# Performance work log

Measured on AMD Instinct MI355X. Metric: run time of the kernel, lower is better.

The kernel has to match this reference:

```python
import jax, jax.numpy as jnp
import numpy as np

N = 100000   # nodes
E = 3200000  # edges
NC = 32


def cheb_conv(x, row, col, W, b):
    """PyG ChebConv with sym normalization and default lambda_max=2.
    Scaled Laplacian L_hat = 2L/lambda_max - I has zero diagonal and
    off-diagonal weights -d_i^{-1/2} d_j^{-1/2} (self-loops removed first).
    W: [K, in, out], b: [out] or None.
    """
    n = x.shape[0]
    ew = jnp.where(row != col, 1.0, 0.0).astype(x.dtype)  # remove_self_loops
    deg = jax.ops.segment_sum(ew, row, num_segments=n)
    dinv = jnp.where(deg > 0, jax.lax.rsqrt(jnp.maximum(deg, 1e-12)), 0.0)
    w = -ew * dinv[row] * dinv[col]  # [E] edge weights of L_hat

    def L(v):  # L_hat @ v via gather + segment-sum scatter
        return jax.ops.segment_sum(w[:, None] * v[col], row, num_segments=n)

    K = W.shape[0]
    Tx0 = x
    out = Tx0 @ W[0]
    if K > 1:
        Tx1 = L(x)
        out = out + Tx1 @ W[1]
        for k in range(2, K):  # Chebyshev recurrence T_k = 2 L T_{k-1} - T_{k-2}
            Tx2 = 2.0 * L(Tx1) - Tx0
            out = out + Tx2 @ W[k]
            Tx0, Tx1 = Tx1, Tx2
    if b is not None:
        out = out + b
    return out


def setup_inputs() -> dict:
    key = jax.random.key(0)
    ks = jax.random.split(key, 10)
    x = jax.random.normal(ks[0], (N, 3), dtype=jnp.float32)
    edge_index = jax.random.randint(ks[1], (2, E), 0, N, dtype=jnp.int64)
    batch = jnp.zeros((N,), dtype=jnp.int64)
    edge_attr = jax.random.normal(ks[2], (E, 1), dtype=jnp.float32)
    s = 0.1
    W1 = jax.random.normal(ks[3], (24, 3, NC), dtype=jnp.float32) * s
    b1 = jnp.zeros((NC,), dtype=jnp.float32)
    W2 = jax.random.normal(ks[4], (12, NC, NC), dtype=jnp.float32) * s
    b2 = jnp.zeros((NC,), dtype=jnp.float32)
    W3 = jax.random.normal(ks[5], (10, NC, NC), dtype=jnp.float32) * s
    b3 = jnp.zeros((NC,), dtype=jnp.float32)
    W4 = jax.random.normal(ks[6], (1, NC, 1), dtype=jnp.float32) * s
    return {"x": x, "edge_index": edge_index, "batch": batch, "edge_attr": edge_attr,
            "W1": W1, "b1": b1, "W2": W2, "b2": b2, "W3": W3, "b3": b3, "W4": W4}


def reference(x, edge_index, batch, edge_attr, W1, b1, W2, b2, W3, b3, W4):
    # batch and edge_attr are unused by ChebNet.forward (kept for signature parity)
    row, col = edge_index[0], edge_index[1]
    h = jax.nn.silu(cheb_conv(x, row, col, W1, b1))
    h = jax.nn.silu(cheb_conv(h, row, col, W2, b2))
    h = jax.nn.silu(cheb_conv(h, row, col, W3, b3))
    return cheb_conv(h, row, col, W4, None)  # block4: K=1, bias=False
```

## Files before the change

kernel.cpp:

```cpp
#include <hip/hip_runtime.h>
#include <math.h>

#define NN 100000
#define EE 3200000
#define NCH 32
#define CAP 96
#define HB 3200256

typedef unsigned short ushortT;
typedef unsigned int uintT;

__device__ __forceinline__ ushortT f2b(float f) {
  uintT u = __float_as_uint(f);
  uintT r = u + 0x7fffu + ((u >> 16) & 1u);
  return (ushortT)(r >> 16);
}
__device__ __forceinline__ uintT pack2(float x, float y) {
  return (uintT)f2b(x) | ((uintT)f2b(y) << 16);
}
__device__ __forceinline__ float lo2f(uintT u) { return __uint_as_float(u << 16); }
__device__ __forceinline__ float hi2f(uintT u) { return __uint_as_float(u & 0xffff0000u); }
__device__ __forceinline__ float silu(float v) { return v / (1.f + expf(-v)); }


__global__ void init_cursor_k(int* __restrict__ cur) {
  int i = blockIdx.x * blockDim.x + threadIdx.x;
  if (i < NN) cur[i] = i * CAP;
}

__global__ void fill_all_k(const int* __restrict__ ei, int* __restrict__ cursor,
                           int* __restrict__ colc) {
  int b = blockIdx.x;
  int w = b & 7;
  int t = (b >> 3) * 256 + threadIdx.x;
  if (t * 4 >= EE) return;
  int step = (NN + 7) / 8;
  int lo = w * step;
  int hi = lo + step < NN ? lo + step : NN;
  int4 r4 = ((const int4*)ei)[t];
  bool i0 = r4.x >= lo && r4.x < hi;
  bool i1 = r4.y >= lo && r4.y < hi;
  bool i2 = r4.z >= lo && r4.z < hi;
  bool i3 = r4.w >= lo && r4.w < hi;
  if (!(i0 | i1 | i2 | i3)) return;
  int4 c4 = ((const int4*)(ei + EE))[t];
  if (i0 && r4.x != c4.x) colc[atomicAdd(&cursor[r4.x], 1)] = c4.x;
  if (i1 && r4.y != c4.y) colc[atomicAdd(&cursor[r4.y], 1)] = c4.y;
  if (i2 && r4.z != c4.z) colc[atomicAdd(&cursor[r4.z], 1)] = c4.z;
  if (i3 && r4.w != c4.w) colc[atomicAdd(&cursor[r4.w], 1)] = c4.w;
}

__global__ __launch_bounds__(256) void prep_k(
    const int* __restrict__ rend, const float* __restrict__ x,
    float* __restrict__ dinv, float* __restrict__ d2, float* __restrict__ sqd,
    uint2* __restrict__ Vfb) {
  if (blockIdx.x == 0 && threadIdx.x < 24)
    Vfb[(size_t)threadIdx.x * (NN + 1) + NN] = make_uint2(0u, 0u);
  int i = blockIdx.x * blockDim.x + threadIdx.x;
  if (i >= NN) return;
  int c = rend[i] - i * CAP;
  float di = (c > 0) ? rsqrtf((float)c) : 0.f;
  dinv[i] = di;
  d2[i] = di * di;
  sqd[i] = (c > 0) ? sqrtf((float)c) : 1.f;
  Vfb[i] = make_uint2(pack2(di * x[3 * i], di * x[3 * i + 1]),
                      pack2(di * x[3 * i + 2], 0.f));
}

__global__ void sent_b16_k(uintT* __restrict__ Vh0, uintT* __restrict__ Vh1,
                           char* __restrict__ R) {
  int t = threadIdx.x;
  int tb = t >> 3, d = t & 7;
  if (tb >= 14) return;
  uintT* base;
  if (tb == 12) base = Vh0;
  else if (tb == 13) base = Vh1;
  else base = (uintT*)(R + (size_t)tb * HB);
  base[(size_t)NN * 8 + d] = 0u;
}


template <bool FIRST>
__global__ __launch_bounds__(256) void cheb_f3_k(
    const int* __restrict__ rend, const int* __restrict__ colc,
    const float* __restrict__ d2, const uint2* __restrict__ U,
    const uint2* __restrict__ A, uint2* __restrict__ Vo) {
  int t8 = blockIdx.x * blockDim.x + threadIdx.x;
  int i = t8 >> 3, q = t8 & 7;
  if (i >= NN) return;
  int s = i * CAP, e = rend[i];
  float a0 = 0.f, a1 = 0.f, a2 = 0.f;
  for (int b = s; b < e; b += 32) {
    int4 cq = *(const int4*)(colc + b + 4 * q);
    int eb = b + 4 * q;
    int c0 = (eb + 0 < e) ? cq.x : NN;
    int c1 = (eb + 1 < e) ? cq.y : NN;
    int c2 = (eb + 2 < e) ? cq.z : NN;
    int c3 = (eb + 3 < e) ? cq.w : NN;
    uint2 r0 = U[c0], r1 = U[c1], r2 = U[c2], r3 = U[c3];
    a0 += lo2f(r0.x); a1 += hi2f(r0.x); a2 += lo2f(r0.y);
    a0 += lo2f(r1.x); a1 += hi2f(r1.x); a2 += lo2f(r1.y);
    a0 += lo2f(r2.x); a1 += hi2f(r2.x); a2 += lo2f(r2.y);
    a0 += lo2f(r3.x); a1 += hi2f(r3.x); a2 += lo2f(r3.y);
  }
  a0 += __shfl_xor(a0, 1); a1 += __shfl_xor(a1, 1); a2 += __shfl_xor(a2, 1);
  a0 += __shfl_xor(a0, 2); a1 += __shfl_xor(a1, 2); a2 += __shfl_xor(a2, 2);
  a0 += __shfl_xor(a0, 4); a1 += __shfl_xor(a1, 4); a2 += __shfl_xor(a2, 4);
  if (q == 0) {
    float d2i = d2[i];
    float v0, v1, v2;
    if (FIRST) {
      v0 = -d2i * a0; v1 = -d2i * a1; v2 = -d2i * a2;
    } else {
      uint2 ap = A[i];
      v0 = fmaf(-2.f * d2i, a0, -lo2f(ap.x));
      v1 = fmaf(-2.f * d2i, a1, -hi2f(ap.x));
      v2 = fmaf(-2.f * d2i, a2, -lo2f(ap.y));
    }
    Vo[i] = make_uint2(pack2(v0, v1), pack2(v2, 0.f));
  }
}

template <int K0, int K1>
__device__ __forceinline__ void sum_planes(const uint2* __restrict__ Vfb, int i,
                                           const float* __restrict__ W1,
                                           float* __restrict__ s_) {
#pragma unroll
  for (int k = K0; k < K1; ++k) {
    uint2 u = Vfb[(size_t)k * (NN + 1) + i];
    float v0 = lo2f(u.x), v1 = hi2f(u.x), v2 = lo2f(u.y);
    const float* Wk = W1 + k * 96;
#pragma unroll
    for (int j = 0; j < 32; ++j)
      s_[j] = fmaf(v0, Wk[j], fmaf(v1, Wk[32 + j], fmaf(v2, Wk[64 + j], s_[j])));
  }
}

__global__ __launch_bounds__(256) void gemm_l1_k(
    const float* __restrict__ x, const uint2* __restrict__ Vfb,
    const float* __restrict__ W1, const float* __restrict__ b1,
    const float* __restrict__ dinv, const float* __restrict__ sqd,
    ushortT* __restrict__ Vh0, ushortT* __restrict__ Vh1) {
  __shared__ float red[4 * 64 * 36];
  int tid = threadIdx.x;
  int w = tid >> 6, lane = tid & 63;
  int i = blockIdx.x * 64 + lane;
  float s_[32];
#pragma unroll
  for (int j = 0; j < 32; ++j) s_[j] = 0.f;
  if (i < NN) {
    if (w == 0) sum_planes<1, 7>(Vfb, i, W1, s_);
    else if (w == 1) sum_planes<7, 13>(Vfb, i, W1, s_);
    else if (w == 2) sum_planes<13, 19>(Vfb, i, W1, s_);
    else sum_planes<19, 24>(Vfb, i, W1, s_);
  }
  float* rb = &red[(w * 64 + lane) * 36];
#pragma unroll
  for (int j = 0; j < 32; ++j) rb[j] = s_[j];
  __syncthreads();
  int r = tid >> 2, q = tid & 3;
  int io = blockIdx.x * 64 + r;
  if (io >= NN) return;
  float acc8[8];
#pragma unroll
  for (int c = 0; c < 8; ++c) acc8[c] = 0.f;
#pragma unroll
  for (int ww = 0; ww < 4; ++ww) {
    const float* p = &red[(ww * 64 + r) * 36 + q * 8];
#pragma unroll
    for (int c = 0; c < 8; ++c) acc8[c] += p[c];
  }
  float x0 = x[3 * io], x1 = x[3 * io + 1], x2 = x[3 * io + 2];
  float sq = sqd[io], di = dinv[io];
  uintT o[4];
#pragma unroll
  for (int cp = 0; cp < 4; ++cp) {
    int j0 = q * 8 + 2 * cp, j1 = j0 + 1;
    float g0 = fmaf(sq, acc8[2 * cp],
        fmaf(x0, W1[j0], fmaf(x1, W1[32 + j0], fmaf(x2, W1[64 + j0], b1[j0]))));
    float g1 = fmaf(sq, acc8[2 * cp + 1],
        fmaf(x0, W1[j1], fmaf(x1, W1[32 + j1], fmaf(x2, W1[64 + j1], b1[j1]))));
    o[cp] = pack2(di * silu(g0), di * silu(g1));
  }
  uintT* dst = (uintT*)((q >> 1) ? Vh1 : Vh0) + (size_t)io * 8 + (q & 1) * 4;
  *(uint4*)dst = make_uint4(o[0], o[1], o[2], o[3]);
}


template <bool FIRST>
__global__ __launch_bounds__(256, 4) void cheb_x_k(
    const int* __restrict__ rend, const int* __restrict__ colc,
    const float* __restrict__ d2,
    const uint4* __restrict__ U0, const uint4* __restrict__ U1,
    const uint4* __restrict__ Ap0, const uint4* __restrict__ Ap1,
    uint4* __restrict__ Vo0, uint4* __restrict__ Vo1) {
  int b = blockIdx.x;
  int xcd = b & 7;
  int h = xcd >> 2;
  int sub = (b >> 3) * 4 + (xcd & 3);
  int t = sub * 256 + threadIdx.x;
  int i = t >> 2;
  if (i >= NN) return;
  const uint4* U = h ? U1 : U0;
  const uint4* Ap = h ? Ap1 : Ap0;
  uint4* Vo = h ? Vo1 : Vo0;
  int g = t & 3;
  int slot = g & 1, h2 = g >> 1;
  int lb = (threadIdx.x & 63) & 60;
  int s = i * CAP, e = rend[i];
  float a0 = 0.f, a1 = 0.f, a2 = 0.f, a3 = 0.f;
  float a4 = 0.f, a5 = 0.f, a6 = 0.f, a7 = 0.f;
  for (int bb = s; bb < e; bb += 16) {
    int4 cq = *(const int4*)(colc + bb + 4 * g);
    int sl0 = lb + 2 * h2, sl1 = sl0 + 1;
    int eb = bb + 8 * h2;
    int c0 = __shfl(cq.x, sl0), c1 = __shfl(cq.y, sl0);
    int c2 = __shfl(cq.z, sl0), c3 = __shfl(cq.w, sl0);
    int c4 = __shfl(cq.x, sl1), c5 = __shfl(cq.y, sl1);
    int c6 = __shfl(cq.z, sl1), c7 = __shfl(cq.w, sl1);
    c0 = (eb + 0 < e) ? c0 : NN;
    c1 = (eb + 1 < e) ? c1 : NN;
    c2 = (eb + 2 < e) ? c2 : NN;
    c3 = (eb + 3 < e) ? c3 : NN;
    c4 = (eb + 4 < e) ? c4 : NN;
    c5 = (eb + 5 < e) ? c5 : NN;
    c6 = (eb + 6 < e) ? c6 : NN;
    c7 = (eb + 7 < e) ? c7 : NN;
    uint4 r0 = U[(size_t)c0 * 2 + slot];
    uint4 r1 = U[(size_t)c1 * 2 + slot];
    uint4 r2 = U[(size_t)c2 * 2 + slot];
    uint4 r3 = U[(size_t)c3 * 2 + slot];
    uint4 r4 = U[(size_t)c4 * 2 + slot];
    uint4 r5 = U[(size_t)c5 * 2 + slot];
    uint4 r6 = U[(size_t)c6 * 2 + slot];
    uint4 r7 = U[(size_t)c7 * 2 + slot];
    a0 += lo2f(r0.x); a1 += hi2f(r0.x); a2 += lo2f(r0.y); a3 += hi2f(r0.y);
    a4 += lo2f(r0.z); a5 += hi2f(r0.z); a6 += lo2f(r0.w); a7 += hi2f(r0.w);
    a0 += lo2f(r1.x); a1 += hi2f(r1.x); a2 += lo2f(r1.y); a3 += hi2f(r1.y);
    a4 += lo2f(r1.z); a5 += hi2f(r1.z); a6 += lo2f(r1.w); a7 += hi2f(r1.w);
    a0 += lo2f(r2.x); a1 += hi2f(r2.x); a2 += lo2f(r2.y); a3 += hi2f(r2.y);
    a4 += lo2f(r2.z); a5 += hi2f(r2.z); a6 += lo2f(r2.w); a7 += hi2f(r2.w);
    a0 += lo2f(r3.x); a1 += hi2f(r3.x); a2 += lo2f(r3.y); a3 += hi2f(r3.y);
    a4 += lo2f(r3.z); a5 += hi2f(r3.z); a6 += lo2f(r3.w); a7 += hi2f(r3.w);
    a0 += lo2f(r4.x); a1 += hi2f(r4.x); a2 += lo2f(r4.y); a3 += hi2f(r4.y);
    a4 += lo2f(r4.z); a5 += hi2f(r4.z); a6 += lo2f(r4.w); a7 += hi2f(r4.w);
    a0 += lo2f(r5.x); a1 += hi2f(r5.x); a2 += lo2f(r5.y); a3 += hi2f(r5.y);
    a4 += lo2f(r5.z); a5 += hi2f(r5.z); a6 += lo2f(r5.w); a7 += hi2f(r5.w);
    a0 += lo2f(r6.x); a1 += hi2f(r6.x); a2 += lo2f(r6.y); a3 += hi2f(r6.y);
    a4 += lo2f(r6.z); a5 += hi2f(r6.z); a6 += lo2f(r6.w); a7 += hi2f(r6.w);
    a0 += lo2f(r7.x); a1 += hi2f(r7.x); a2 += lo2f(r7.y); a3 += hi2f(r7.y);
    a4 += lo2f(r7.z); a5 += hi2f(r7.z); a6 += lo2f(r7.w); a7 += hi2f(r7.w);
  }
  a0 += __shfl_xor(a0, 2); a1 += __shfl_xor(a1, 2);
  a2 += __shfl_xor(a2, 2); a3 += __shfl_xor(a3, 2);
  a4 += __shfl_xor(a4, 2); a5 += __shfl_xor(a5, 2);
  a6 += __shfl_xor(a6, 2); a7 += __shfl_xor(a7, 2);
  if (g >= 2) return;
  float d2i = d2[i];
  float v0, v1, v2, v3, v4, v5, v6, v7;
  if (FIRST) {
    v0 = -d2i * a0; v1 = -d2i * a1; v2 = -d2i * a2; v3 = -d2i * a3;
    v4 = -d2i * a4; v5 = -d2i * a5; v6 = -d2i * a6; v7 = -d2i * a7;
  } else {
    uint4 au = Ap[(size_t)i * 2 + slot];
    v0 = fmaf(-2.f * d2i, a0, -lo2f(au.x));
    v1 = fmaf(-2.f * d2i, a1, -hi2f(au.x));
    v2 = fmaf(-2.f * d2i, a2, -lo2f(au.y));
    v3 = fmaf(-2.f * d2i, a3, -hi2f(au.y));
    v4 = fmaf(-2.f * d2i, a4, -lo2f(au.z));
    v5 = fmaf(-2.f * d2i, a5, -hi2f(au.z));
    v6 = fmaf(-2.f * d2i, a6, -lo2f(au.w));
    v7 = fmaf(-2.f * d2i, a7, -hi2f(au.w));
  }
  Vo[(size_t)i * 2 + slot] = make_uint4(pack2(v0, v1), pack2(v2, v3),
                                        pack2(v4, v5), pack2(v6, v7));
}

__device__ __forceinline__ void fma_pair(uintT dw, const float* __restrict__ Wc,
                                         float a[32]) {
  float vl = lo2f(dw), vh = hi2f(dw);
#pragma unroll
  for (int j = 0; j < 32; ++j) a[j] = fmaf(vl, Wc[j], a[j]);
#pragma unroll
  for (int j = 0; j < 32; ++j) a[j] = fmaf(vh, Wc[32 + j], a[j]);
}

__device__ __forceinline__ void fma_plane(uint4 u0, uint4 u1, uint4 u2, uint4 u3,
                                          const float* __restrict__ W,
                                          float a[32]) {
  fma_pair(u0.x, W + 0 * 64, a);   fma_pair(u0.y, W + 1 * 64, a);
  fma_pair(u0.z, W + 2 * 64, a);   fma_pair(u0.w, W + 3 * 64, a);
  fma_pair(u1.x, W + 4 * 64, a);   fma_pair(u1.y, W + 5 * 64, a);
  fma_pair(u1.z, W + 6 * 64, a);   fma_pair(u1.w, W + 7 * 64, a);
  fma_pair(u2.x, W + 8 * 64, a);   fma_pair(u2.y, W + 9 * 64, a);
  fma_pair(u2.z, W + 10 * 64, a);  fma_pair(u2.w, W + 11 * 64, a);
  fma_pair(u3.x, W + 12 * 64, a);  fma_pair(u3.y, W + 13 * 64, a);
  fma_pair(u3.z, W + 14 * 64, a);  fma_pair(u3.w, W + 15 * 64, a);
}

template <int NP, bool INIT, int EPI>
__global__ __launch_bounds__(256, 2) void gemm_r_k(
    const uintT* __restrict__ A0, const uintT* __restrict__ A1,
    const uintT* __restrict__ B0, const uintT* __restrict__ B1,
    const uintT* __restrict__ C0, const uintT* __restrict__ C1,
    const uintT* __restrict__ D0, const uintT* __restrict__ D1,
    const float* __restrict__ W, float* __restrict__ acc,
    const float* __restrict__ bb, const float* __restrict__ sqd,
    const float* __restrict__ dinv, const float* __restrict__ W4,
    ushortT* __restrict__ Vh0, ushortT* __restrict__ Vh1,
    float* __restrict__ out) {
  int i = blockIdx.x * blockDim.x + threadIdx.x;
  if (i >= NN) return;
  uint4 ua0, ua1, ua2, ua3, ub0, ub1, ub2, ub3;
  uint4 uc0, uc1, uc2, uc3, ud0, ud1, ud2, ud3;
  {
    const uint4* p0 = (const uint4*)(A0 + (size_t)i * 8);
    const uint4* p1 = (const uint4*)(A1 + (size_t)i * 8);
    ua0 = p0[0]; ua1 = p0[1]; ua2 = p1[0]; ua3 = p1[1];
  }
  if (NP >= 2) {
    const uint4* p0 = (const uint4*)(B0 + (size_t)i * 8);
    const uint4* p1 = (const uint4*)(B1 + (size_t)i * 8);
    ub0 = p0[0]; ub1 = p0[1]; ub2 = p1[0]; ub3 = p1[1];
  }
  if (NP >= 3) {
    const uint4* p0 = (const uint4*)(C0 + (size_t)i * 8);
    const uint4* p1 = (const uint4*)(C1 + (size_t)i * 8);
    uc0 = p0[0]; uc1 = p0[1]; uc2 = p1[0]; uc3 = p1[1];
  }
  if (NP >= 4) {
    const uint4* p0 = (const uint4*)(D0 + (size_t)i * 8);
    const uint4* p1 = (const uint4*)(D1 + (size_t)i * 8);
    ud0 = p0[0]; ud1 = p0[1]; ud2 = p1[0]; ud3 = p1[1];
  }
  float a[32];
  if (INIT) {
#pragma unroll
    for (int j = 0; j < 32; ++j) a[j] = 0.f;
  } else {
    const float4* ar = (const float4*)(acc + (size_t)i * 32);
#pragma unroll
    for (int q = 0; q < 8; ++q) {
      float4 v = ar[q];
      a[4 * q] = v.x; a[4 * q + 1] = v.y; a[4 * q + 2] = v.z; a[4 * q + 3] = v.w;
    }
  }
  fma_plane(ua0, ua1, ua2, ua3, W, a);
  if (NP >= 2) fma_plane(ub0, ub1, ub2, ub3, W + 1024, a);
  if (NP >= 3) fma_plane(uc0, uc1, uc2, uc3, W + 2048, a);
  if (NP >= 4) fma_plane(ud0, ud1, ud2, ud3, W + 3072, a);
  if (EPI == 0) {
    float4* ar = (float4*)(acc + (size_t)i * 32);
#pragma unroll
    for (int q = 0; q < 8; ++q)
      ar[q] = make_float4(a[4 * q], a[4 * q + 1], a[4 * q + 2], a[4 * q + 3]);
  } else if (EPI == 1) {
    float sq = sqd[i], di = dinv[i];
    uintT o[16];
#pragma unroll
    for (int p = 0; p < 16; ++p) {
      float g0 = fmaf(sq, a[2 * p], bb[2 * p]);
      float g1 = fmaf(sq, a[2 * p + 1], bb[2 * p + 1]);
      o[p] = pack2(di * silu(g0), di * silu(g1));
    }
    uintT* w0 = (uintT*)Vh0 + (size_t)i * 8;
    uintT* w1 = (uintT*)Vh1 + (size_t)i * 8;
    *(uint4*)w0 = make_uint4(o[0], o[1], o[2], o[3]);
    *(uint4*)(w0 + 4) = make_uint4(o[4], o[5], o[6], o[7]);
    *(uint4*)w1 = make_uint4(o[8], o[9], o[10], o[11]);
    *(uint4*)(w1 + 4) = make_uint4(o[12], o[13], o[14], o[15]);
  } else {
    float sq = sqd[i];
    float g = 0.f;
#pragma unroll
    for (int j = 0; j < 32; ++j)
      g = fmaf(silu(fmaf(sq, a[j], bb[j])), W4[j], g);
    out[i] = g;
  }
}


extern "C" void kernel_launch(void* const* d_in, const int* in_sizes, int n_in,
                              void* d_out, int out_size, void* d_ws, size_t ws_size,
                              hipStream_t stream) {
  const float* x = (const float*)d_in[0];
  const int* ei = (const int*)d_in[1];
  const float* W1 = (const float*)d_in[4];
  const float* b1 = (const float*)d_in[5];
  const float* W2 = (const float*)d_in[6];
  const float* b2 = (const float*)d_in[7];
  const float* W3 = (const float*)d_in[8];
  const float* b3 = (const float*)d_in[9];
  const float* W4 = (const float*)d_in[10];
  float* out = (float*)d_out;

  char* ws = (char*)d_ws;
  size_t off = 0;
  auto alloc = [&](size_t bytes) {
    void* p = ws + off;
    off += (bytes + 255) & ~(size_t)255;
    return p;
  };
  int* rend = (int*)alloc((size_t)NN * 4);
  float* dinv = (float*)alloc((size_t)NN * 4);
  float* d2 = (float*)alloc((size_t)NN * 4);
  float* sqd = (float*)alloc((size_t)NN * 4);
  int* colc = (int*)alloc((size_t)NN * CAP * 4 + 128);
  ushortT* Vh0 = (ushortT*)alloc(HB);
  ushortT* Vh1 = (ushortT*)alloc(HB);
  float* acc = (float*)alloc((size_t)NN * NCH * 4);
  char* R = (char*)alloc((size_t)12 * HB);
  uint2* Vfb = (uint2*)R;
  (void)ws_size; (void)in_sizes; (void)n_in; (void)out_size;

  const int GR = (NN + 255) / 256;
  const int GR8 = (NN * 8 + 255) / 256;
  const int GL1 = (NN + 63) / 64;
  const int GX = 3200;

  init_cursor_k<<<GR, 256, 0, stream>>>(rend);
  fill_all_k<<<8 * (EE / 4 / 256), 256, 0, stream>>>(ei, rend, colc);
  prep_k<<<GR, 256, 0, stream>>>(rend, x, dinv, d2, sqd, Vfb);

  auto Vp = [&](int k) { return Vfb + (size_t)k * (NN + 1); };
  cheb_f3_k<true><<<GR8, 256, 0, stream>>>(rend, colc, d2, Vp(0), nullptr, Vp(1));
  for (int k = 2; k < 24; ++k)
    cheb_f3_k<false><<<GR8, 256, 0, stream>>>(rend, colc, d2, Vp(k - 1), Vp(k - 2), Vp(k));
  gemm_l1_k<<<GL1, 256, 0, stream>>>(x, Vfb, W1, b1, dinv, sqd, Vh0, Vh1);

  sent_b16_k<<<1, 128, 0, stream>>>((uintT*)Vh0, (uintT*)Vh1, R);
  auto Rh = [&](int k, int h) {
    return (uintT*)(R + (size_t)(((k - 1) % 6) * 2 + h) * HB);
  };
  auto cheb_step = [&](int k) {
    const uint4* U0 = (const uint4*)((k == 1) ? (uintT*)Vh0 : Rh(k - 1, 0));
    const uint4* U1 = (const uint4*)((k == 1) ? (uintT*)Vh1 : Rh(k - 1, 1));
    if (k == 1) {
      cheb_x_k<true><<<GX, 256, 0, stream>>>(rend, colc, d2, U0, U1,
                                             nullptr, nullptr,
                                             (uint4*)Rh(k, 0), (uint4*)Rh(k, 1));
    } else {
      const uint4* A0 = (const uint4*)((k == 2) ? (uintT*)Vh0 : Rh(k - 2, 0));
      const uint4* A1 = (const uint4*)((k == 2) ? (uintT*)Vh1 : Rh(k - 2, 1));
      cheb_x_k<false><<<GX, 256, 0, stream>>>(rend, colc, d2, U0, U1, A0, A1,
                                              (uint4*)Rh(k, 0), (uint4*)Rh(k, 1));
    }
  };

  {
    const float* W = W2;
    for (int k = 1; k < 12; ++k) {
      cheb_step(k);
      if (k == 2)
        gemm_r_k<3, true, 0><<<GR, 256, 0, stream>>>(
            (uintT*)Vh0, (uintT*)Vh1, Rh(1, 0), Rh(1, 1), Rh(2, 0), Rh(2, 1),
            nullptr, nullptr, W, acc,
            nullptr, nullptr, nullptr, nullptr, nullptr, nullptr, nullptr);
      else if (k == 5)
        gemm_r_k<3, false, 0><<<GR, 256, 0, stream>>>(
            Rh(3, 0), Rh(3, 1), Rh(4, 0), Rh(4, 1), Rh(5, 0), Rh(5, 1),
            nullptr, nullptr, W + 3 * 1024, acc,
            nullptr, nullptr, nullptr, nullptr, nullptr, nullptr, nullptr);
      else if (k == 8)
        gemm_r_k<3, false, 0><<<GR, 256, 0, stream>>>(
            Rh(6, 0), Rh(6, 1), Rh(7, 0), Rh(7, 1), Rh(8, 0), Rh(8, 1),
            nullptr, nullptr, W + 6 * 1024, acc,
            nullptr, nullptr, nullptr, nullptr, nullptr, nullptr, nullptr);
    }
    gemm_r_k<3, false, 1><<<GR, 256, 0, stream>>>(
        Rh(9, 0), Rh(9, 1), Rh(10, 0), Rh(10, 1), Rh(11, 0), Rh(11, 1),
        nullptr, nullptr, W + 9 * 1024, acc,
        b2, sqd, dinv, nullptr, Vh0, Vh1, nullptr);
  }

  {
    const float* W = W3;
    for (int k = 1; k < 10; ++k) {
      cheb_step(k);
      if (k == 2)
        gemm_r_k<3, true, 0><<<GR, 256, 0, stream>>>(
            (uintT*)Vh0, (uintT*)Vh1, Rh(1, 0), Rh(1, 1), Rh(2, 0), Rh(2, 1),
            nullptr, nullptr, W, acc,
            nullptr, nullptr, nullptr, nullptr, nullptr, nullptr, nullptr);
      else if (k == 5)
        gemm_r_k<3, false, 0><<<GR, 256, 0, stream>>>(
            Rh(3, 0), Rh(3, 1), Rh(4, 0), Rh(4, 1), Rh(5, 0), Rh(5, 1),
            nullptr, nullptr, W + 3 * 1024, acc,
            nullptr, nullptr, nullptr, nullptr, nullptr, nullptr, nullptr);
    }
    gemm_r_k<4, false, 2><<<GR, 256, 0, stream>>>(
        Rh(6, 0), Rh(6, 1), Rh(7, 0), Rh(7, 1), Rh(8, 0), Rh(8, 1),
        Rh(9, 0), Rh(9, 1), W + 6 * 1024, acc,
        b3, sqd, nullptr, W4, nullptr, nullptr, out);
  }
}
```

Measured before the change: 1.656 ms.

## Split dense GEMM output columns across blocks and regroup Chebyshev terms per launch

Adds gemm_rs_k, which splits the 32 output channels into two halves handled by separate blocks (16 accumulators per thread). This raises parallelism and cuts register pressure in the per-node dense projection. The GEMM launches are regrouped to handle four Chebyshev terms each instead of three, so there are fewer launches and fewer accumulator round-trips. Occupancy hints on the sparse propagation kernels are also raised, which risks register spills. The split re-reads each node's input features once per half, doubling that read traffic.

```diff
diff --git a/kernel.cpp b/kernel.cpp
--- a/kernel.cpp
+++ b/kernel.cpp
@@ -81,7 +81,7 @@
 
 
 template <bool FIRST>
-__global__ __launch_bounds__(256) void cheb_f3_k(
+__global__ __launch_bounds__(256, 8) void cheb_f3_k(
     const int* __restrict__ rend, const int* __restrict__ colc,
     const float* __restrict__ d2, const uint2* __restrict__ U,
     const uint2* __restrict__ A, uint2* __restrict__ Vo) {
@@ -188,7 +188,7 @@
 
 
 template <bool FIRST>
-__global__ __launch_bounds__(256, 4) void cheb_x_k(
+__global__ __launch_bounds__(256, 6) void cheb_x_k(
     const int* __restrict__ rend, const int* __restrict__ colc,
     const float* __restrict__ d2,
     const uint4* __restrict__ U0, const uint4* __restrict__ U1,
@@ -284,7 +284,6 @@
 #pragma unroll
   for (int j = 0; j < 32; ++j) a[j] = fmaf(vh, Wc[32 + j], a[j]);
 }
-
 __device__ __forceinline__ void fma_plane(uint4 u0, uint4 u1, uint4 u2, uint4 u3,
                                           const float* __restrict__ W,
                                           float a[32]) {
@@ -303,13 +302,91 @@
     const uintT* __restrict__ A0, const uintT* __restrict__ A1,
     const uintT* __restrict__ B0, const uintT* __restrict__ B1,
     const uintT* __restrict__ C0, const uintT* __restrict__ C1,
+    const float* __restrict__ W, float* __restrict__ acc,
+    const float* __restrict__ bb, const float* __restrict__ sqd,
+    const float* __restrict__ W4, float* __restrict__ out) {
+  int i = blockIdx.x * blockDim.x + threadIdx.x;
+  if (i >= NN) return;
+  uint4 ua0, ua1, ua2, ua3, ub0, ub1, ub2, ub3, uc0, uc1, uc2, uc3;
+  {
+    const uint4* p0 = (const uint4*)(A0 + (size_t)i * 8);
+    const uint4* p1 = (const uint4*)(A1 + (size_t)i * 8);
+    ua0 = p0[0]; ua1 = p0[1]; ua2 = p1[0]; ua3 = p1[1];
+  }
+  if (NP >= 2) {
+    const uint4* p0 = (const uint4*)(B0 + (size_t)i * 8);
+    const uint4* p1 = (const uint4*)(B1 + (size_t)i * 8);
+    ub0 = p0[0]; ub1 = p0[1]; ub2 = p1[0]; ub3 = p1[1];
+  }
+  if (NP >= 3) {
+    const uint4* p0 = (const uint4*)(C0 + (size_t)i * 8);
+    const uint4* p1 = (const uint4*)(C1 + (size_t)i * 8);
+    uc0 = p0[0]; uc1 = p0[1]; uc2 = p1[0]; uc3 = p1[1];
+  }
+  float a[32];
+  if (INIT) {
+#pragma unroll
+    for (int j = 0; j < 32; ++j) a[j] = 0.f;
+  } else {
+    const float4* ar = (const float4*)(acc + (size_t)i * 32);
+#pragma unroll
+    for (int q = 0; q < 8; ++q) {
+      float4 v = ar[q];
+      a[4 * q] = v.x; a[4 * q + 1] = v.y; a[4 * q + 2] = v.z; a[4 * q + 3] = v.w;
+    }
+  }
+  fma_plane(ua0, ua1, ua2, ua3, W, a);
+  if (NP >= 2) fma_plane(ub0, ub1, ub2, ub3, W + 1024, a);
+  if (NP >= 3) fma_plane(uc0, uc1, uc2, uc3, W + 2048, a);
+  if (EPI == 2) {
+    float sq = sqd[i];
+    float g = 0.f;
+#pragma unroll
+    for (int j = 0; j < 32; ++j)
+      g = fmaf(silu(fmaf(sq, a[j], bb[j])), W4[j], g);
+    out[i] = g;
+  } else {
+    float4* ar = (float4*)(acc + (size_t)i * 32);
+#pragma unroll
+    for (int q = 0; q < 8; ++q)
+      ar[q] = make_float4(a[4 * q], a[4 * q + 1], a[4 * q + 2], a[4 * q + 3]);
+  }
+}
+
+__device__ __forceinline__ void fma_pair16(uintT dw, const float* __restrict__ Wc,
+                                           float a[16]) {
+  float vl = lo2f(dw), vh = hi2f(dw);
+#pragma unroll
+  for (int j = 0; j < 16; ++j) a[j] = fmaf(vl, Wc[j], a[j]);
+#pragma unroll
+  for (int j = 0; j < 16; ++j) a[j] = fmaf(vh, Wc[32 + j], a[j]);
+}
+__device__ __forceinline__ void fma_plane16(uint4 u0, uint4 u1, uint4 u2, uint4 u3,
+                                            const float* __restrict__ W,
+                                            float a[16]) {
+  fma_pair16(u0.x, W + 0 * 64, a);   fma_pair16(u0.y, W + 1 * 64, a);
+  fma_pair16(u0.z, W + 2 * 64, a);   fma_pair16(u0.w, W + 3 * 64, a);
+  fma_pair16(u1.x, W + 4 * 64, a);   fma_pair16(u1.y, W + 5 * 64, a);
+  fma_pair16(u1.z, W + 6 * 64, a);   fma_pair16(u1.w, W + 7 * 64, a);
+  fma_pair16(u2.x, W + 8 * 64, a);   fma_pair16(u2.y, W + 9 * 64, a);
+  fma_pair16(u2.z, W + 10 * 64, a);  fma_pair16(u2.w, W + 11 * 64, a);
+  fma_pair16(u3.x, W + 12 * 64, a);  fma_pair16(u3.y, W + 13 * 64, a);
+  fma_pair16(u3.z, W + 14 * 64, a);  fma_pair16(u3.w, W + 15 * 64, a);
+}
+
+template <int NP, bool INIT, int EPI>
+__global__ __launch_bounds__(256, 2) void gemm_rs_k(
+    const uintT* __restrict__ A0, const uintT* __restrict__ A1,
+    const uintT* __restrict__ B0, const uintT* __restrict__ B1,
+    const uintT* __restrict__ C0, const uintT* __restrict__ C1,
     const uintT* __restrict__ D0, const uintT* __restrict__ D1,
     const float* __restrict__ W, float* __restrict__ acc,
     const float* __restrict__ bb, const float* __restrict__ sqd,
-    const float* __restrict__ dinv, const float* __restrict__ W4,
-    ushortT* __restrict__ Vh0, ushortT* __restrict__ Vh1,
-    float* __restrict__ out) {
-  int i = blockIdx.x * blockDim.x + threadIdx.x;
+    const float* __restrict__ dinv,
+    ushortT* __restrict__ Vh0, ushortT* __restrict__ Vh1) {
+  int bid = blockIdx.x;
+  int jh = bid & 1;
+  int i = (bid >> 1) * 256 + threadIdx.x;
   if (i >= NN) return;
   uint4 ua0, ua1, ua2, ua3, ub0, ub1, ub2, ub3;
   uint4 uc0, uc1, uc2, uc3, ud0, ud1, ud2, ud3;
@@ -333,49 +410,40 @@
     const uint4* p1 = (const uint4*)(D1 + (size_t)i * 8);
     ud0 = p0[0]; ud1 = p0[1]; ud2 = p1[0]; ud3 = p1[1];
   }
-  float a[32];
+  const float* Wb = W + jh * 16;
+  float a[16];
   if (INIT) {
 #pragma unroll
-    for (int j = 0; j < 32; ++j) a[j] = 0.f;
+    for (int j = 0; j < 16; ++j) a[j] = 0.f;
   } else {
-    const float4* ar = (const float4*)(acc + (size_t)i * 32);
-#pragma unroll
-    for (int q = 0; q < 8; ++q) {
+    const float4* ar = (const float4*)(acc + (size_t)i * 32 + jh * 16);
+#pragma unroll
+    for (int q = 0; q < 4; ++q) {
       float4 v = ar[q];
       a[4 * q] = v.x; a[4 * q + 1] = v.y; a[4 * q + 2] = v.z; a[4 * q + 3] = v.w;
     }
   }
-  fma_plane(ua0, ua1, ua2, ua3, W, a);
-  if (NP >= 2) fma_plane(ub0, ub1, ub2, ub3, W + 1024, a);
-  if (NP >= 3) fma_plane(uc0, uc1, uc2, uc3, W + 2048, a);
-  if (NP >= 4) fma_plane(ud0, ud1, ud2, ud3, W + 3072, a);
+  fma_plane16(ua0, ua1, ua2, ua3, Wb, a);
+  if (NP >= 2) fma_plane16(ub0, ub1, ub2, ub3, Wb + 1024, a);
+  if (NP >= 3) fma_plane16(uc0, uc1, uc2, uc3, Wb + 2048, a);
+  if (NP >= 4) fma_plane16(ud0, ud1, ud2, ud3, Wb + 3072, a);
   if (EPI == 0) {
-    float4* ar = (float4*)(acc + (size_t)i * 32);
-#pragma unroll
-    for (int q = 0; q < 8; ++q)
+    float4* ar = (float4*)(acc + (size_t)i * 32 + jh * 16);
+#pragma unroll
+    for (int q = 0; q < 4; ++q)
       ar[q] = make_float4(a[4 * q], a[4 * q + 1], a[4 * q + 2], a[4 * q + 3]);
-  } else if (EPI == 1) {
+  } else {
     float sq = sqd[i], di = dinv[i];
-    uintT o[16];
-#pragma unroll
-    for (int p = 0; p < 16; ++p) {
-      float g0 = fmaf(sq, a[2 * p], bb[2 * p]);
-      float g1 = fmaf(sq, a[2 * p + 1], bb[2 * p + 1]);
+    uintT o[8];
+#pragma unroll
+    for (int p = 0; p < 8; ++p) {
+      float g0 = fmaf(sq, a[2 * p], bb[jh * 16 + 2 * p]);
+      float g1 = fmaf(sq, a[2 * p + 1], bb[jh * 16 + 2 * p + 1]);
       o[p] = pack2(di * silu(g0), di * silu(g1));
     }
-    uintT* w0 = (uintT*)Vh0 + (size_t)i * 8;
-    uintT* w1 = (uintT*)Vh1 + (size_t)i * 8;
+    uintT* w0 = (uintT*)(jh ? Vh1 : Vh0) + (size_t)i * 8;
     *(uint4*)w0 = make_uint4(o[0], o[1], o[2], o[3]);
     *(uint4*)(w0 + 4) = make_uint4(o[4], o[5], o[6], o[7]);
-    *(uint4*)w1 = make_uint4(o[8], o[9], o[10], o[11]);
-    *(uint4*)(w1 + 4) = make_uint4(o[12], o[13], o[14], o[15]);
-  } else {
-    float sq = sqd[i];
-    float g = 0.f;
-#pragma unroll
-    for (int j = 0; j < 32; ++j)
-      g = fmaf(silu(fmaf(sq, a[j], bb[j])), W4[j], g);
-    out[i] = g;
   }
 }
 
@@ -417,6 +485,7 @@
   const int GR8 = (NN * 8 + 255) / 256;
   const int GL1 = (NN + 63) / 64;
   const int GX = 3200;
+  const int GS = 2 * GR;
 
   init_cursor_k<<<GR, 256, 0, stream>>>(rend);
   fill_all_k<<<8 * (EE / 4 / 256), 256, 0, stream>>>(ei, rend, colc);
@@ -451,46 +520,39 @@
     const float* W = W2;
     for (int k = 1; k < 12; ++k) {
       cheb_step(k);
-      if (k == 2)
-        gemm_r_k<3, true, 0><<<GR, 256, 0, stream>>>(
+      if (k == 3)
+        gemm_rs_k<4, true, 0><<<GS, 256, 0, stream>>>(
             (uintT*)Vh0, (uintT*)Vh1, Rh(1, 0), Rh(1, 1), Rh(2, 0), Rh(2, 1),
-            nullptr, nullptr, W, acc,
-            nullptr, nullptr, nullptr, nullptr, nullptr, nullptr, nullptr);
-      else if (k == 5)
-        gemm_r_k<3, false, 0><<<GR, 256, 0, stream>>>(
-            Rh(3, 0), Rh(3, 1), Rh(4, 0), Rh(4, 1), Rh(5, 0), Rh(5, 1),
-            nullptr, nullptr, W + 3 * 1024, acc,
-            nullptr, nullptr, nullptr, nullptr, nullptr, nullptr, nullptr);
-      else if (k == 8)
-        gemm_r_k<3, false, 0><<<GR, 256, 0, stream>>>(
-            Rh(6, 0), Rh(6, 1), Rh(7, 0), Rh(7, 1), Rh(8, 0), Rh(8, 1),
-            nullptr, nullptr, W + 6 * 1024, acc,
-            nullptr, nullptr, nullptr, nullptr, nullptr, nullptr, nullptr);
-    }
-    gemm_r_k<3, false, 1><<<GR, 256, 0, stream>>>(
-        Rh(9, 0), Rh(9, 1), Rh(10, 0), Rh(10, 1), Rh(11, 0), Rh(11, 1),
-        nullptr, nullptr, W + 9 * 1024, acc,
-        b2, sqd, dinv, nullptr, Vh0, Vh1, nullptr);
+            Rh(3, 0), Rh(3, 1), W, acc, nullptr, nullptr, nullptr,
+            nullptr, nullptr);
+      else if (k == 7)
+        gemm_rs_k<4, false, 0><<<GS, 256, 0, stream>>>(
+            Rh(4, 0), Rh(4, 1), Rh(5, 0), Rh(5, 1), Rh(6, 0), Rh(6, 1),
+            Rh(7, 0), Rh(7, 1), W + 4 * 1024, acc, nullptr, nullptr, nullptr,
+            nullptr, nullptr);
+    }
+    gemm_rs_k<4, false, 1><<<GS, 256, 0, stream>>>(
+        Rh(8, 0), Rh(8, 1), Rh(9, 0), Rh(9, 1), Rh(10, 0), Rh(10, 1),
+        Rh(11, 0), Rh(11, 1), W + 8 * 1024, acc, b2, sqd, dinv, Vh0, Vh1);
   }
 
   {
     const float* W = W3;
     for (int k = 1; k < 10; ++k) {
       cheb_step(k);
-      if (k == 2)
-        gemm_r_k<3, true, 0><<<GR, 256, 0, stream>>>(
+      if (k == 3)
+        gemm_rs_k<4, true, 0><<<GS, 256, 0, stream>>>(
             (uintT*)Vh0, (uintT*)Vh1, Rh(1, 0), Rh(1, 1), Rh(2, 0), Rh(2, 1),
-            nullptr, nullptr, W, acc,
-            nullptr, nullptr, nullptr, nullptr, nullptr, nullptr, nullptr);
-      else if (k == 5)
-        gemm_r_k<3, false, 0><<<GR, 256, 0, stream>>>(
-            Rh(3, 0), Rh(3, 1), Rh(4, 0), Rh(4, 1), Rh(5, 0), Rh(5, 1),
-            nullptr, nullptr, W + 3 * 1024, acc,
-            nullptr, nullptr, nullptr, nullptr, nullptr, nullptr, nullptr);
-    }
-    gemm_r_k<4, false, 2><<<GR, 256, 0, stream>>>(
-        Rh(6, 0), Rh(6, 1), Rh(7, 0), Rh(7, 1), Rh(8, 0), Rh(8, 1),
-        Rh(9, 0), Rh(9, 1), W + 6 * 1024, acc,
-        b3, sqd, nullptr, W4, nullptr, nullptr, out);
-  }
-}
+            Rh(3, 0), Rh(3, 1), W, acc, nullptr, nullptr, nullptr,
+            nullptr, nullptr);
+      else if (k == 6)
+        gemm_rs_k<3, false, 0><<<GS, 256, 0, stream>>>(
+            Rh(4, 0), Rh(4, 1), Rh(5, 0), Rh(5, 1), Rh(6, 0), Rh(6, 1),
+            nullptr, nullptr, W + 4 * 1024, acc, nullptr, nullptr, nullptr,
+            nullptr, nullptr);
+    }
+    gemm_r_k<3, false, 2><<<GR, 256, 0, stream>>>(
+        Rh(7, 0), Rh(7, 1), Rh(8, 0), Rh(8, 1), Rh(9, 0), Rh(9, 1),
+        W + 7 * 1024, acc, b3, sqd, W4, out);
+  }
+}
```

Measured after the change: 1.533 ms. 7.4% less time.
